# Kernel tuning notes

Hardware: AMD Instinct MI355X
Metric: run time of the kernel (lower is better)

## Reference

```python
import jax, jax.numpy as jnp
import numpy as np

EPS = 1e-6  # LayerNorm epsilon


def setup_inputs() -> dict:
    key = jax.random.key(0)
    ks = jax.random.split(key, 12)
    B, S, T, E = 8, 2048, 2048, 512
    sc = 1.0 / np.sqrt(E)
    inp = {
        "encoder_outputs": jax.random.normal(ks[0], (B, S, E), jnp.float32),
        "emotion": jax.random.normal(ks[1], (B, T, E), jnp.float32),
        "mask": jax.random.randint(ks[2], (B, S, T), 0, 2).astype(bool),
        "Wq": jax.random.normal(ks[3], (E, E), jnp.float32) * sc,
        "bq": jnp.zeros((E,), jnp.float32),
        "Wk": jax.random.normal(ks[4], (E, E), jnp.float32) * sc,
        "bk": jnp.zeros((E,), jnp.float32),
        "Wv": jax.random.normal(ks[5], (E, E), jnp.float32) * sc,
        "bv": jnp.zeros((E,), jnp.float32),
        "Wo": jax.random.normal(ks[6], (E, E), jnp.float32) * sc,
        "gamma": jnp.ones((E,), jnp.float32),
        "beta": jnp.zeros((E,), jnp.float32),
    }
    return inp


def reference(encoder_outputs, emotion, mask, Wq, bq, Wk, bk, Wv, bv, Wo, gamma, beta):
    # Linear projections (torch Linear: x @ W.T + b)
    q = encoder_outputs @ Wq.T + bq          # [B,S,E]
    k = emotion @ Wk.T + bk                  # [B,T,E]
    v = emotion @ Wv.T + bv                  # [B,T,E]
    logits = jnp.einsum("bse,bte->bst", q, k)  # [B,S,T]
    logits = jnp.where(mask, jnp.float32(-1e18), logits)
    weights = jax.nn.softmax(logits, axis=-1)   # dropout1 = identity (eval)
    contexts = jnp.einsum("bst,bte->bse", weights, v)
    attn = contexts @ Wo.T                   # output_linear, no bias
    attn = encoder_outputs + attn            # dropout2 = identity (eval)
    # LayerNorm (std-based, as in common hand-rolled LayerNorm)
    mean = attn.mean(-1, keepdims=True)
    std = attn.std(-1, keepdims=True)
    context = gamma * (attn - mean) / (std + EPS) + beta
    context = encoder_outputs + context      # dropout3 = identity (eval)
    return context
```

## Files before the change

### kernel.cpp

```cpp
#include <hip/hip_runtime.h>
#include <math.h>
#include <stdint.h>


#define BB 8
#define SS 2048
#define TT 2048
#define EE 512

typedef __attribute__((ext_vector_type(8))) short short8;
typedef __attribute__((ext_vector_type(4))) float f32x4;

__device__ __forceinline__ uint16_t f2bf(float f) {
  uint32_t u = __builtin_bit_cast(uint32_t, f);
  u += 0x7fffu + ((u >> 16) & 1u);
  return (uint16_t)(u >> 16);
}
__device__ __forceinline__ float bf2f(uint16_t h) {
  uint32_t u = ((uint32_t)h) << 16;
  return __builtin_bit_cast(float, u);
}

__device__ __forceinline__ size_t toff(int row, int col, int ld) {
  return (size_t)(row >> 4) * ((size_t)ld << 4) + ((size_t)(col >> 3) << 7)
       + ((row & 15) << 3) + (col & 7);
}

__device__ __forceinline__ void gld16(const void* g, void* l) {
  __builtin_amdgcn_global_load_lds(
      (const __attribute__((address_space(1))) void*)g,
      (__attribute__((address_space(3))) void*)l, 16, 0, 0);
}

template<int ASRC, int BSRC, int EPI, int WN>
__global__ __launch_bounds__(256, 2) void mgemm(
    const void* __restrict__ Ap, const void* __restrict__ Alo,
    const void* __restrict__ Bp, const void* __restrict__ Blo,
    void* __restrict__ Cp, void* __restrict__ C2,
    const float* __restrict__ bias, const float* __restrict__ bias2,
    const float* __restrict__ resid,
    const int* __restrict__ mask, float* __restrict__ sZ,
    int K, int lda, int ldb, int ldc,
    size_t sA, size_t sB, size_t sC, size_t sM)
{
  constexpr bool ALOARR = (ASRC == 0);
  constexpr bool BLOARR = (BSRC == 0);
  constexpr bool T3     = (ASRC == 0) && (BSRC == 0);
  constexpr bool T2     = (ASRC == 0) && (BSRC == 1);
  constexpr int  BN     = 32 * WN;
  constexpr int  ABYTES = ALOARR ? 16384 : 8192;
  constexpr int  BBYTES = BLOARR ? BN * 128 : BN * 64;

  __shared__ char smem[ABYTES + BBYTES];

  const int tid  = threadIdx.x;
  const int lane = tid & 63, wv = tid >> 6;
  const int z    = blockIdx.z;
  const int bm   = blockIdx.y * 128;
  const int bn   = blockIdx.x * BN;
  const int fr   = lane & 15;
  const int wm   = (wv & 1) * 64;
  const int wn   = (wv >> 1) * (16 * WN);

  const f32x4 zero = {0.f, 0.f, 0.f, 0.f};
  f32x4 acc[4][WN];
#pragma unroll
  for (int i = 0; i < 4; ++i)
#pragma unroll
    for (int j = 0; j < WN; ++j) acc[i][j] = zero;

  const size_t loff = (size_t)lane * 8;
  const uint16_t* gAh = (const uint16_t*)Ap + sA * z + (size_t)(bm >> 4) * 16 * lda + loff;
  const uint16_t* gAl = ALOARR ? (const uint16_t*)Alo + sA * z + (size_t)(bm >> 4) * 16 * lda + loff : nullptr;
  const uint16_t* gBh = (const uint16_t*)Bp + sB * z + (size_t)(bn >> 4) * 16 * ldb + loff;
  const uint16_t* gBl = BLOARR ? (const uint16_t*)Blo + sB * z + (size_t)(bn >> 4) * 16 * ldb + loff : nullptr;

  for (int k0 = 0; k0 < K; k0 += 32) {
    const size_t ka = (size_t)k0 * 16;
    __syncthreads();
#pragma unroll
    for (int t = 0; t < 2; ++t) { int s = wv + t * 4;
      gld16(gAh + (size_t)s * 16 * lda + ka, &smem[s * 1024]); }
    if constexpr (ALOARR) {
#pragma unroll
      for (int t = 0; t < 2; ++t) { int s = wv + t * 4;
        gld16(gAl + (size_t)s * 16 * lda + ka, &smem[8192 + s * 1024]); }
    }
#pragma unroll
    for (int t = 0; t < WN / 2; ++t) { int s = wv + t * 4;
      gld16(gBh + (size_t)s * 16 * ldb + ka, &smem[ABYTES + s * 1024]); }
    if constexpr (BLOARR) {
#pragma unroll
      for (int t = 0; t < WN / 2; ++t) { int s = wv + t * 4;
        gld16(gBl + (size_t)s * 16 * ldb + ka, &smem[ABYTES + BN * 64 + s * 1024]); }
    }
    __syncthreads();

    short8 ah[4], bh[WN], al_[4], bl_[WN];
#pragma unroll
    for (int i = 0; i < 4; ++i) {
      const char* p = smem + ((wm >> 4) + i) * 1024 + (lane << 4);
      ah[i] = *(const short8*)p;
      if constexpr (ALOARR) al_[i] = *(const short8*)(p + 8192);
    }
#pragma unroll
    for (int j = 0; j < WN; ++j) {
      const char* p = smem + ABYTES + ((wn >> 4) + j) * 1024 + (lane << 4);
      bh[j] = *(const short8*)p;
      if constexpr (BLOARR) bl_[j] = *(const short8*)(p + BN * 64);
    }
#pragma unroll
    for (int i = 0; i < 4; ++i)
#pragma unroll
      for (int j = 0; j < WN; ++j) {
        acc[i][j] = __builtin_amdgcn_mfma_f32_16x16x32_bf16(ah[i], bh[j], acc[i][j], 0, 0, 0);
        if constexpr (T3) {
          acc[i][j] = __builtin_amdgcn_mfma_f32_16x16x32_bf16(ah[i], bl_[j], acc[i][j], 0, 0, 0);
          acc[i][j] = __builtin_amdgcn_mfma_f32_16x16x32_bf16(al_[i], bh[j], acc[i][j], 0, 0, 0);
        } else if constexpr (T2) {
          acc[i][j] = __builtin_amdgcn_mfma_f32_16x16x32_bf16(al_[i], bh[j], acc[i][j], 0, 0, 0);
        }
      }
  }

  if constexpr (EPI == 5) {
    const unsigned long long* __restrict__ mb = (const unsigned long long*)mask;
    const size_t mrow = (size_t)TT >> 6;
    const size_t mbase = (size_t)z * SS * mrow + ((size_t)(bn + wn) >> 6);
    unsigned long long mw[4][4];
#pragma unroll
    for (int i = 0; i < 4; ++i)
#pragma unroll
      for (int g = 0; g < 4; ++g) {
        const int row = bm + wm + i * 16 + (lane >> 4) * 4 + g;
        mw[i][g] = mb[mbase + (size_t)row * mrow];
      }
#pragma unroll
    for (int i = 0; i < 4; ++i) {
      const int row0 = bm + wm + i * 16 + (lane >> 4) * 4;
#pragma unroll
      for (int g = 0; g < 4; ++g) {
        const int row = row0 + g;
        float rs = 0.f;
#pragma unroll
        for (int j = 0; j < WN; ++j) {
          const int col = bn + wn + j * 16 + fr;
          const bool msk = (mw[i][g] >> (j * 16 + fr)) & 1ull;
          const float e = msk ? 0.f : __expf(acc[i][j][g] - 60.0f);
          ((uint16_t*)Cp)[sC * z + toff(row, col, ldc)] = f2bf(e);
          rs += e;
        }
        rs += __shfl_xor(rs, 1);
        rs += __shfl_xor(rs, 2);
        rs += __shfl_xor(rs, 4);
        rs += __shfl_xor(rs, 8);
        if ((lane & 15) == 0) atomicAdd(&sZ[(size_t)z * SS + row], rs);
      }
    }
  } else {
#pragma unroll
    for (int i = 0; i < 4; ++i) {
      const int row0 = bm + wm + i * 16 + (lane >> 4) * 4;
#pragma unroll
      for (int g = 0; g < 4; ++g) {
        const int row = row0 + g;
        float invZ = 1.0f;
        if constexpr (EPI == 6) invZ = 1.0f / sZ[(size_t)z * SS + row];
#pragma unroll
        for (int j = 0; j < WN; ++j) {
          const int col = bn + wn + j * 16 + fr;
          float v = acc[i][j][g];
          if constexpr (EPI == 0) {
            const float* bp = (z == 0) ? bias : bias2;
            const size_t ci = sC * z + toff(row, col, ldc);
            v += bp[col];
            uint16_t h = f2bf(v);
            ((uint16_t*)Cp)[ci] = h;
            if (z == 0) ((uint16_t*)C2)[ci] = f2bf(v - bf2f(h));
          } else if constexpr (EPI == 1) {
            v += bias[row];
            ((uint16_t*)Cp)[sC * z + toff(row, col, ldc)] = f2bf(v);
          } else if constexpr (EPI == 4) {
            v += resid[(size_t)row * ldc + col];
            ((float*)Cp)[sC * z + (size_t)row * ldc + col] = v;
          } else {
            ((uint16_t*)Cp)[sC * z + toff(row, col, ldc)] = f2bf(v * invZ);
          }
        }
      }
    }
  }
}

__device__ __forceinline__ void split_core(
    const float* __restrict__ x, uint16_t* __restrict__ hi,
    uint16_t* __restrict__ lo, int bid)
{
  __shared__ uint16_t lh[256 * 8 + 16 * 8];
  __shared__ uint16_t ll[256 * 8 + 16 * 8];
  const int t   = threadIdx.x;
  const int seg = bid >> 2, q = bid & 3;

  const float* src = x + (size_t)(seg * 16 + (t >> 4)) * 512 + q * 128 + (t & 15) * 8;
  float4 a = *(const float4*)src;
  float4 b = *(const float4*)(src + 4);
  float v[8] = {a.x, a.y, a.z, a.w, b.x, b.y, b.z, b.w};

  const int slot = (t & 15) * 16 + (t >> 4);
  uint16_t* ph = lh + slot * 8 + (slot >> 4) * 8;
  uint16_t* pl = ll + slot * 8 + (slot >> 4) * 8;
#pragma unroll
  for (int e = 0; e < 8; ++e) {
    uint16_t h = f2bf(v[e]);
    ph[e] = h;
    pl[e] = f2bf(v[e] - bf2f(h));
  }
  __syncthreads();

  const uint16_t* qh = lh + t * 8 + (t >> 4) * 8;
  const uint16_t* ql = ll + t * 8 + (t >> 4) * 8;
  const size_t off = (size_t)seg * 8192 + (size_t)(q * 16 + (t >> 4)) * 128 + (t & 15) * 8;
  *(short8*)(hi + off) = *(const short8*)qh;
  *(short8*)(lo + off) = *(const short8*)ql;
}

__global__ __launch_bounds__(256) void split_pair(
    const float* __restrict__ x0, const float* __restrict__ x1,
    uint16_t* __restrict__ hi, uint16_t* __restrict__ lo, size_t stride,
    const int* __restrict__ mask, unsigned long long* __restrict__ mbits)
{
  if (blockIdx.x >= 8192) {
    const int lane = threadIdx.x & 63;
    const size_t wvid = ((size_t)(blockIdx.x - 8192) * 256 + threadIdx.x) >> 6;
    const size_t w = wvid * 64 + lane;
    const int4* mp = (const int4*)mask + (w << 4);
    unsigned long long bits = 0;
#pragma unroll
    for (int j = 0; j < 16; ++j) {
      const int4 m = mp[j];
      const unsigned nib = (unsigned)(m.x != 0) | ((unsigned)(m.y != 0) << 1)
                         | ((unsigned)(m.z != 0) << 2) | ((unsigned)(m.w != 0) << 3);
      bits |= (unsigned long long)nib << (j * 4);
    }
    mbits[w] = bits;
    return;
  }
  const int sel = blockIdx.x >> 12;
  const int bid = blockIdx.x & 4095;
  split_core(sel ? x1 : x0, hi + sel * stride, lo + sel * stride, bid);
}

__global__ __launch_bounds__(256) void split_w4(
    const float* __restrict__ x0, const float* __restrict__ x1,
    const float* __restrict__ x2, const float* __restrict__ x3,
    uint16_t* __restrict__ hi0, uint16_t* __restrict__ lo0, size_t stride)
{
  const int w   = blockIdx.x >> 7;
  const int bid = blockIdx.x & 127;
  const float* x = (w == 0) ? x0 : (w == 1) ? x1 : (w == 2) ? x2 : x3;
  split_core(x, hi0 + w * stride, lo0 + w * stride, bid);
}

__global__ __launch_bounds__(256) void ln_kernel(
    const float* __restrict__ X, const float* __restrict__ enc,
    const float* __restrict__ gamma, const float* __restrict__ beta,
    float* __restrict__ out)
{
  const int row = blockIdx.x * 4 + (threadIdx.x >> 6);
  const int lane = threadIdx.x & 63;
  const size_t base = (size_t)row * EE;
  const int o0 = lane * 4, o1 = 256 + lane * 4;

  float4 x0 = *(const float4*)(X + base + o0);
  float4 x1 = *(const float4*)(X + base + o1);
  float s = x0.x + x0.y + x0.z + x0.w + x1.x + x1.y + x1.z + x1.w;
#pragma unroll
  for (int off = 32; off > 0; off >>= 1) s += __shfl_xor(s, off);
  const float mean = s * (1.0f / 512.0f);

  float d[8] = {x0.x - mean, x0.y - mean, x0.z - mean, x0.w - mean,
                x1.x - mean, x1.y - mean, x1.z - mean, x1.w - mean};
  float s2 = 0.f;
#pragma unroll
  for (int i = 0; i < 8; ++i) s2 = fmaf(d[i], d[i], s2);
#pragma unroll
  for (int off = 32; off > 0; off >>= 1) s2 += __shfl_xor(s2, off);
  const float stdv = sqrtf(s2 * (1.0f / 512.0f));
  const float inv = 1.0f / (stdv + 1e-6f);

  float4 g0 = *(const float4*)(gamma + o0);
  float4 g1 = *(const float4*)(gamma + o1);
  float4 b0 = *(const float4*)(beta + o0);
  float4 b1 = *(const float4*)(beta + o1);
  float4 e0 = *(const float4*)(enc + base + o0);
  float4 e1 = *(const float4*)(enc + base + o1);

  float4 r0, r1;
  r0.x = e0.x + g0.x * d[0] * inv + b0.x;
  r0.y = e0.y + g0.y * d[1] * inv + b0.y;
  r0.z = e0.z + g0.z * d[2] * inv + b0.z;
  r0.w = e0.w + g0.w * d[3] * inv + b0.w;
  r1.x = e1.x + g1.x * d[4] * inv + b1.x;
  r1.y = e1.y + g1.y * d[5] * inv + b1.y;
  r1.z = e1.z + g1.z * d[6] * inv + b1.z;
  r1.w = e1.w + g1.w * d[7] * inv + b1.w;
  *(float4*)(out + base + o0) = r0;
  *(float4*)(out + base + o1) = r1;
}

extern "C" void kernel_launch(void* const* d_in, const int* in_sizes, int n_in,
                              void* d_out, int out_size, void* d_ws, size_t ws_size,
                              hipStream_t stream) {
  const float* enc   = (const float*)d_in[0];
  const float* emo   = (const float*)d_in[1];
  const int*   mask  = (const int*)d_in[2];
  const float* Wq    = (const float*)d_in[3];
  const float* bq    = (const float*)d_in[4];
  const float* Wk    = (const float*)d_in[5];
  const float* bk    = (const float*)d_in[6];
  const float* Wv    = (const float*)d_in[7];
  const float* bv    = (const float*)d_in[8];
  const float* Wo    = (const float*)d_in[9];
  const float* gamma = (const float*)d_in[10];
  const float* beta  = (const float*)d_in[11];
  float* out = (float*)d_out;
  char*  ws  = (char*)d_ws;

  const size_t SZ = (size_t)BB * SS * EE;
  size_t off = 0;
  uint16_t* enc_h = (uint16_t*)(ws + off); off += SZ * 2;
  uint16_t* enc_l = (uint16_t*)(ws + off); off += SZ * 2;
  uint16_t* emo_h = (uint16_t*)(ws + off); off += SZ * 2;
  uint16_t* emo_l = (uint16_t*)(ws + off); off += SZ * 2;
  uint16_t* q_hi  = (uint16_t*)(ws + off); off += SZ * 2;
  uint16_t* q_lo  = (uint16_t*)(ws + off); off += SZ * 2;
  uint16_t* k_hi  = (uint16_t*)(ws + off); off += SZ * 2;
  uint16_t* k_lo  = (uint16_t*)(ws + off); off += SZ * 2;
  uint16_t* vT    = (uint16_t*)(ws + off); off += SZ * 2;
  uint16_t* ctx   = (uint16_t*)(ws + off); off += SZ * 2;
  uint16_t* wq_h  = (uint16_t*)(ws + off); off += EE * EE * 2;
  uint16_t* wq_l  = (uint16_t*)(ws + off); off += EE * EE * 2;
  uint16_t* wk_h  = (uint16_t*)(ws + off); off += EE * EE * 2;
  uint16_t* wk_l  = (uint16_t*)(ws + off); off += EE * EE * 2;
  uint16_t* wv_h  = (uint16_t*)(ws + off); off += EE * EE * 2;
  uint16_t* wv_l  = (uint16_t*)(ws + off); off += EE * EE * 2;
  uint16_t* wo_h  = (uint16_t*)(ws + off); off += EE * EE * 2;
  uint16_t* wo_l  = (uint16_t*)(ws + off); off += EE * EE * 2;
  uint16_t* P_u   = (uint16_t*)(ws + off); off += (size_t)BB * SS * TT * 2;
  float*    sZ    = (float*)(ws + off);    off += (size_t)BB * SS * 4;
  (void)wk_l; (void)wv_l; (void)wo_l;

  unsigned long long* mbits = (unsigned long long*)k_lo;

  const dim3 blk(256);

  split_w4<<<dim3(512), blk, 0, stream>>>(Wq, Wk, Wv, Wo, wq_h, wq_l,
                                          (size_t)2 * EE * EE);
  split_pair<<<dim3(8192 + 2048), blk, 0, stream>>>(enc, emo, enc_h, enc_l,
                                                    (size_t)2 * SZ, mask, mbits);
  hipMemsetAsync(sZ, 0, (size_t)BB * SS * 4, stream);

  mgemm<0, 0, 0, 4><<<dim3(4, 128, 2), blk, 0, stream>>>(
      enc_h, enc_l, wq_h, wq_l, q_hi, q_lo, bq, bk, nullptr, nullptr, nullptr,
      EE, EE, EE, EE, 2 * SZ, (size_t)2 * EE * EE, 2 * SZ, 0);
  mgemm<1, 1, 1, 4><<<dim3(128, 4, 1), blk, 0, stream>>>(
      wv_h, nullptr, emo_h, nullptr, vT, nullptr, bv, nullptr, nullptr,
      nullptr, nullptr, EE, EE, EE, BB * TT, 0, 0, 0, 0);

  mgemm<0, 1, 5, 4><<<dim3(16, 16, 8), blk, 0, stream>>>(
      q_hi, q_lo, k_hi, nullptr, P_u, nullptr, nullptr, nullptr, nullptr,
      (const int*)mbits, sZ, EE, EE, EE, TT,
      (size_t)SS * EE, (size_t)TT * EE, (size_t)SS * TT, 0);

  mgemm<1, 1, 6, 4><<<dim3(4, 16, 8), blk, 0, stream>>>(
      P_u, nullptr, vT, nullptr, ctx, nullptr, nullptr, nullptr, nullptr,
      nullptr, sZ, TT, TT, BB * TT, EE,
      (size_t)SS * TT, (size_t)TT * 16, (size_t)SS * EE, 0);

  mgemm<1, 1, 4, 4><<<dim3(4, 128, 1), blk, 0, stream>>>(
      ctx, nullptr, wo_h, nullptr, out, nullptr, nullptr, nullptr, enc,
      nullptr, nullptr, EE, EE, EE, EE, 0, 0, 0, 0);
  ln_kernel<<<dim3(BB * SS / 4), blk, 0, stream>>>(out, enc, gamma, beta, out);
}
```

Measured before the change: 541.0 us.

## Fuse input bf16 split and mask bit-packing into one register-only prepass

Replaces the split_pair kernel, which staged data through shared memory with a barrier and launched separate blocks for mask packing, with one prepass kernel of 2048 blocks. Each thread converts two 16-float chunks directly into hi/lo bf16 tiles with vector stores and then packs one 64-bit mask word, so every block mixes both jobs. The aim is to cut LDS traffic, the __syncthreads and the block count for this memory-bound pre-processing. In exchange the per-thread global access pattern changes, and it must still match the tiled layout exactly.

```diff
diff --git a/kernel.cpp b/kernel.cpp
--- a/kernel.cpp
+++ b/kernel.cpp
@@ -224,30 +224,69 @@
   *(short8*)(lo + off) = *(const short8*)ql;
 }
 
-__global__ __launch_bounds__(256) void split_pair(
-    const float* __restrict__ x0, const float* __restrict__ x1,
+__global__ __launch_bounds__(256) void prepass(
+    const float* __restrict__ enc, const float* __restrict__ emo,
     uint16_t* __restrict__ hi, uint16_t* __restrict__ lo, size_t stride,
     const int* __restrict__ mask, unsigned long long* __restrict__ mbits)
 {
-  if (blockIdx.x >= 8192) {
-    const int lane = threadIdx.x & 63;
-    const size_t wvid = ((size_t)(blockIdx.x - 8192) * 256 + threadIdx.x) >> 6;
-    const size_t w = wvid * 64 + lane;
-    const int4* mp = (const int4*)mask + (w << 4);
-    unsigned long long bits = 0;
-#pragma unroll
-    for (int j = 0; j < 16; ++j) {
-      const int4 m = mp[j];
-      const unsigned nib = (unsigned)(m.x != 0) | ((unsigned)(m.y != 0) << 1)
-                         | ((unsigned)(m.z != 0) << 2) | ((unsigned)(m.w != 0) << 3);
-      bits |= (unsigned long long)nib << (j * 4);
-    }
-    mbits[w] = bits;
-    return;
+  const int tid  = threadIdx.x;
+  const int lane = tid & 63;
+  const int gw   = blockIdx.x * 4 + (tid >> 6);
+  const int lr   = lane & 15;
+  const int lg   = lane >> 4;
+
+#pragma unroll
+  for (int it = 0; it < 2; ++it) {
+    const int t   = gw * 2 + it;
+    const int arr = t >> 13;
+    const int rg  = (t & 8191) >> 3;
+    const int cg  = t & 7;
+    const float* src = (arr ? emo : enc)
+        + (size_t)(rg * 16 + lr) * 512 + cg * 64 + lg * 16;
+    float4 a = *(const float4*)src;
+    float4 b = *(const float4*)(src + 4);
+    float4 c = *(const float4*)(src + 8);
+    float4 d = *(const float4*)(src + 12);
+    float v[16] = {a.x, a.y, a.z, a.w, b.x, b.y, b.z, b.w,
+                   c.x, c.y, c.z, c.w, d.x, d.y, d.z, d.w};
+    short8 h0, h1, l0, l1;
+#pragma unroll
+    for (int e = 0; e < 8; ++e) {
+      uint16_t h = f2bf(v[e]);
+      h0[e] = (short)h; l0[e] = (short)f2bf(v[e] - bf2f(h));
+    }
+#pragma unroll
+    for (int e = 0; e < 8; ++e) {
+      uint16_t h = f2bf(v[8 + e]);
+      h1[e] = (short)h; l1[e] = (short)f2bf(v[8 + e] - bf2f(h));
+    }
+    const size_t off = (size_t)arr * stride + (size_t)rg * 8192
+                     + (size_t)(cg * 8 + lg * 2) * 128 + lr * 8;
+    *(short8*)(hi + off)       = h0;
+    *(short8*)(hi + off + 128) = h1;
+    *(short8*)(lo + off)       = l0;
+    *(short8*)(lo + off + 128) = l1;
   }
-  const int sel = blockIdx.x >> 12;
-  const int bid = blockIdx.x & 4095;
-  split_core(sel ? x1 : x0, hi + sel * stride, lo + sel * stride, bid);
+
+  const size_t w = (size_t)blockIdx.x * 256 + tid;
+  const int4* mp = (const int4*)mask + (w << 4);
+  unsigned long long bits = 0;
+#pragma unroll
+  for (int r = 0; r < 4; ++r) {
+    int4 m0 = mp[r * 4 + 0], m1 = mp[r * 4 + 1];
+    int4 m2 = mp[r * 4 + 2], m3 = mp[r * 4 + 3];
+    unsigned g = 0;
+    g |= (unsigned)(m0.x != 0)       | ((unsigned)(m0.y != 0) << 1)
+       | ((unsigned)(m0.z != 0) << 2) | ((unsigned)(m0.w != 0) << 3);
+    g |= ((unsigned)(m1.x != 0) << 4) | ((unsigned)(m1.y != 0) << 5)
+       | ((unsigned)(m1.z != 0) << 6) | ((unsigned)(m1.w != 0) << 7);
+    g |= ((unsigned)(m2.x != 0) << 8) | ((unsigned)(m2.y != 0) << 9)
+       | ((unsigned)(m2.z != 0) << 10) | ((unsigned)(m2.w != 0) << 11);
+    g |= ((unsigned)(m3.x != 0) << 12) | ((unsigned)(m3.y != 0) << 13)
+       | ((unsigned)(m3.z != 0) << 14) | ((unsigned)(m3.w != 0) << 15);
+    bits |= (unsigned long long)g << (r * 16);
+  }
+  mbits[w] = bits;
 }
 
 __global__ __launch_bounds__(256) void split_w4(
@@ -356,8 +395,8 @@
 
   split_w4<<<dim3(512), blk, 0, stream>>>(Wq, Wk, Wv, Wo, wq_h, wq_l,
                                           (size_t)2 * EE * EE);
-  split_pair<<<dim3(8192 + 2048), blk, 0, stream>>>(enc, emo, enc_h, enc_l,
-                                                    (size_t)2 * SZ, mask, mbits);
+  prepass<<<dim3(2048), blk, 0, stream>>>(enc, emo, enc_h, enc_l,
+                                          (size_t)2 * SZ, mask, mbits);
   hipMemsetAsync(sZ, 0, (size_t)BB * SS * 4, stream);
 
   mgemm<0, 0, 0, 4><<<dim3(4, 128, 2), blk, 0, stream>>>(
```

Result: no change. 543.2 us (+0.4%).
